# Optimization experiments

Hardware: AMD Instinct MI355X
Metric: run time of the kernel (lower is better)

The kernel has to match this reference:

```python
import jax, jax.numpy as jnp
import numpy as np

NUM_AGENT = 200
LOOK_BACK = 10
NUM_CTRL = 9
DIM = 512
HEADS = 8
DIM_HEAD = 64
N = NUM_AGENT * LOOK_BACK + NUM_CTRL  # 2009
BATCH = 4
SCALE = DIM_HEAD ** -0.5


def _build_mask():
    # eye(num_agent) repeat_interleaved by look_back on rows and cols == kron with ones(lb,lb)
    m = jnp.kron(jnp.eye(NUM_AGENT, dtype=jnp.float32),
                 jnp.ones((LOOK_BACK, LOOK_BACK), jnp.float32))
    # pad with zeros for the control-feature rows/cols
    return jnp.pad(m, ((0, NUM_CTRL), (0, NUM_CTRL)))  # [N, N]


def _split_heads(t):
    b, n, hd = t.shape
    return t.reshape(b, n, HEADS, hd // HEADS).transpose(0, 2, 1, 3)  # [b,h,n,d]


def setup_inputs() -> dict:
    key = jax.random.key(0)
    ks = jax.random.split(key, 5)
    inner = HEADS * DIM_HEAD
    return {
        "x": jax.random.normal(ks[0], (BATCH, N, DIM), jnp.float32),
        "w_qkv": jax.random.normal(ks[1], (DIM, inner * 3), jnp.float32) * 0.02,
        "w_qk_self": jax.random.normal(ks[2], (DIM, inner * 2), jnp.float32) * 0.02,
        "w_out": jax.random.normal(ks[3], (inner, DIM), jnp.float32) * 0.02,
        "b_out": jnp.zeros((DIM,), jnp.float32),
    }


def reference(x, w_qkv, w_qk_self, w_out, b_out):
    mask = _build_mask()  # [N, N], broadcasts over [b, h]
    q, k, v = map(_split_heads, jnp.split(x @ w_qkv, 3, axis=-1))
    q_s, k_s = map(_split_heads, jnp.split(x @ w_qk_self, 2, axis=-1))
    dots = jnp.einsum('bhnd,bhmd->bhnm', q, k) * SCALE
    dots_self = jnp.einsum('bhnd,bhmd->bhnm', q_s, k_s) * SCALE
    blended = mask * dots_self + (1.0 - mask) * dots
    attn = jax.nn.softmax(blended, axis=-1)  # [b,h,n,n]
    out = jnp.einsum('bhnm,bhmd->bhnd', attn, v)
    out = out.transpose(0, 2, 1, 3).reshape(x.shape[0], N, HEADS * DIM_HEAD)
    return out @ w_out + b_out, attn
```

## Files before the change

### kernel.cpp

```cpp
#include <hip/hip_runtime.h>
#include <hip/hip_bf16.h>


#define N_TOK   2009
#define NPAD    2048
#define NTILES  16
#define NT2     32
#define BATCH_  4
#define HEADS_  8
#define MROWS   8036
#define SCALE_  0.125f
#define RPB_A   256
#define RPV     128
#define PFP     68

typedef __attribute__((ext_vector_type(8)))  short sh8;
typedef __attribute__((ext_vector_type(16))) float f32x16;

static inline int cdiv(int a, int b) { return (a + b - 1) / b; }

__device__ __forceinline__ float4 ld4(const float* p) {
    return *reinterpret_cast<const float4*>(p);
}
__device__ __forceinline__ unsigned short f2bf(float f) {
    __hip_bfloat16 h = __float2bfloat16(f);
    return *reinterpret_cast<unsigned short*>(&h);
}
__device__ __forceinline__ float bf2f(unsigned short u) {
    return __uint_as_float(((unsigned)u) << 16);
}
__device__ __forceinline__ void cvt8(const float4& a, const float4& b, sh8& hi, sh8& lo) {
    float f[8] = {a.x, a.y, a.z, a.w, b.x, b.y, b.z, b.w};
#pragma unroll
    for (int i = 0; i < 8; ++i) {
        unsigned short h = f2bf(f[i]);
        hi[i] = (short)h;
        lo[i] = (short)f2bf(f[i] - bf2f(h));
    }
}
__device__ __forceinline__ void cvt8p(const float4& a, const float4& b, sh8& hi) {
#pragma unroll
    for (int i = 0; i < 4; ++i) {
        hi[i]     = (short)f2bf((&a.x)[i]);
        hi[4 + i] = (short)f2bf((&b.x)[i]);
    }
}
typedef const __attribute__((address_space(1))) void gas_void;
typedef __attribute__((address_space(3))) void las_void;
__device__ __forceinline__ void gll16(const void* g, void* l) {
    __builtin_amdgcn_global_load_lds((gas_void*)g, (las_void*)l, 16, 0, 0);
}

__device__ __forceinline__ void bar_lds() {
    asm volatile("s_waitcnt lgkmcnt(0)" ::: "memory");
    __builtin_amdgcn_sched_barrier(0);
    __builtin_amdgcn_s_barrier();
    __builtin_amdgcn_sched_barrier(0);
}
__device__ __forceinline__ void bar_keep16() {
    asm volatile("s_waitcnt vmcnt(16) lgkmcnt(0)" ::: "memory");
    __builtin_amdgcn_sched_barrier(0);
    __builtin_amdgcn_s_barrier();
    __builtin_amdgcn_sched_barrier(0);
}

__global__ __launch_bounds__(256)
void convert_x(const float* __restrict__ x, unsigned short* __restrict__ xh,
               unsigned short* __restrict__ xl)
{
    const int mt = blockIdx.x;
    const int yq = blockIdx.y;
    const int w  = threadIdx.x >> 6;
    const int kc = threadIdx.x & 63;
    for (int it = 0; it < 2; ++it) {
        int rg = (yq * 2 + it) * 4 + w;
        sh8 hi[4], lo[4];
#pragma unroll
        for (int rr = 0; rr < 4; ++rr) {
            int row = rg * 4 + rr;
            int gm = mt * 128 + row;
            int b = gm >> 11, gr = gm & 2047;
            float4 a = make_float4(0.f, 0.f, 0.f, 0.f), c = a;
            if (gr < N_TOK) {
                const float* p = x + ((size_t)b * N_TOK + gr) * 512 + kc * 8;
                a = ld4(p); c = ld4(p + 4);
            }
            cvt8(a, c, hi[rr], lo[rr]);
        }
        size_t base = ((size_t)(mt * 64 + kc) * 128 + rg * 4) * 8;
#pragma unroll
        for (int rr = 0; rr < 4; ++rr) {
            *reinterpret_cast<sh8*>(xh + base + rr * 8) = hi[rr];
            *reinterpret_cast<sh8*>(xl + base + rr * 8) = lo[rr];
        }
    }
}

__global__ __launch_bounds__(256)
void convert_w(const float* __restrict__ wqkv, const float* __restrict__ wself,
               const float* __restrict__ wout,
               unsigned short* __restrict__ qh, unsigned short* __restrict__ ql,
               unsigned short* __restrict__ sh, unsigned short* __restrict__ sl,
               unsigned short* __restrict__ oh, unsigned short* __restrict__ ol)
{
    int cid = blockIdx.x * 256 + threadIdx.x;
    int nt_all = cid >> 13, rem = cid & 8191;
    int kc = rem >> 7, col = rem & 127;
    const float* src; unsigned short *dh, *dl; int Nn, ntl;
    if (nt_all < 12)      { src = wqkv;  dh = qh; dl = ql; Nn = 1536; ntl = nt_all; }
    else if (nt_all < 20) { src = wself; dh = sh; dl = sl; Nn = 1024; ntl = nt_all - 12; }
    else                  { src = wout;  dh = oh; dl = ol; Nn = 512;  ntl = nt_all - 20; }
    float f[8];
#pragma unroll
    for (int i = 0; i < 8; ++i)
        f[i] = src[(size_t)(kc * 8 + i) * Nn + ntl * 128 + col];
    sh8 hi, lo;
    cvt8(make_float4(f[0], f[1], f[2], f[3]), make_float4(f[4], f[5], f[6], f[7]), hi, lo);
    size_t off = ((size_t)(ntl * 64 + kc) * 128 + col) * 8;
    *reinterpret_cast<sh8*>(dh + off) = hi;
    *reinterpret_cast<sh8*>(dl + off) = lo;
}

template<int MODE>
__global__ __launch_bounds__(512)
void gemm_bf16(const unsigned short* __restrict__ Ah, const unsigned short* __restrict__ Al,
               const unsigned short* __restrict__ Bh, const unsigned short* __restrict__ Bl,
               float* __restrict__ C, const float* __restrict__ bias)
{
    __shared__ __align__(16) unsigned short AhS[2][4096], AlS[2][4096],
                                            BhS[2][4096], BlS[2][4096];
    const int tid = threadIdx.x, lane = tid & 63, wid = tid >> 6;
    const int mt = blockIdx.x, ntile = blockIdx.y;
    const int wm = wid >> 2, wn = wid & 3;
    const int lj = lane & 31, g = lane >> 5;

    const unsigned short* Asrc_h = Ah + (size_t)mt * 65536;
    const unsigned short* Asrc_l = Al + (size_t)mt * 65536;
    const unsigned short* Bsrc_h = Bh + (size_t)ntile * 65536;
    const unsigned short* Bsrc_l = Bl + (size_t)ntile * 65536;

#define GSTAGE(BUF, S) do {                                                      \
    gll16(Asrc_h + (size_t)(S) * 4096 + tid * 8, (char*)AhS[BUF] + tid * 16);    \
    gll16(Asrc_l + (size_t)(S) * 4096 + tid * 8, (char*)AlS[BUF] + tid * 16);    \
    gll16(Bsrc_h + (size_t)(S) * 4096 + tid * 8, (char*)BhS[BUF] + tid * 16);    \
    gll16(Bsrc_l + (size_t)(S) * 4096 + tid * 8, (char*)BlS[BUF] + tid * 16);    \
} while (0)

    f32x16 acc[2];
#pragma unroll
    for (int i = 0; i < 16; ++i) { acc[0][i] = 0.f; acc[1][i] = 0.f; }

    GSTAGE(0, 0);
    for (int s = 0; s < 16; ++s) {
        const int buf = s & 1;
        __syncthreads();
        if (s + 1 < 16) GSTAGE(buf ^ 1, s + 1);
#pragma unroll
        for (int ks = 0; ks < 2; ++ks) {
            const int kcl = 2 * ks + g;
            sh8 bh = *reinterpret_cast<const sh8*>(BhS[buf] + (kcl * 128 + wn * 32 + lj) * 8);
            sh8 bl = *reinterpret_cast<const sh8*>(BlS[buf] + (kcl * 128 + wn * 32 + lj) * 8);
#pragma unroll
            for (int Mt = 0; Mt < 2; ++Mt) {
                sh8 ah = *reinterpret_cast<const sh8*>(AhS[buf] + (kcl * 128 + wm * 64 + Mt * 32 + lj) * 8);
                sh8 al = *reinterpret_cast<const sh8*>(AlS[buf] + (kcl * 128 + wm * 64 + Mt * 32 + lj) * 8);
                acc[Mt] = __builtin_amdgcn_mfma_f32_32x32x16_bf16(ah, bh, acc[Mt], 0, 0, 0);
                acc[Mt] = __builtin_amdgcn_mfma_f32_32x32x16_bf16(ah, bl, acc[Mt], 0, 0, 0);
                acc[Mt] = __builtin_amdgcn_mfma_f32_32x32x16_bf16(al, bh, acc[Mt], 0, 0, 0);
            }
        }
    }
#undef GSTAGE

#pragma unroll
    for (int Mt = 0; Mt < 2; ++Mt) {
#pragma unroll
        for (int reg = 0; reg < 16; ++reg) {
            int rloc = wm * 64 + Mt * 32 + (reg & 3) + 8 * (reg >> 2) + 4 * g;
            int gm = mt * 128 + rloc;
            int b = gm >> 11, gr = gm & 2047;
            if (gr < N_TOK) {
                int coln = ntile * 128 + wn * 32 + lj;
                float v = acc[Mt][reg];
                size_t idx;
                if (MODE == 1)
                    idx = ((size_t)(coln >> 9) * MROWS + (size_t)b * N_TOK + gr) * 512 + (coln & 511);
                else if (MODE == 0)
                    idx = ((size_t)b * N_TOK + gr) * 1024 + coln;
                else {
                    v += bias[coln];
                    idx = ((size_t)b * N_TOK + gr) * 512 + coln;
                }
                C[idx] = v;
            }
        }
    }
}

__global__ __launch_bounds__(256)
void selfE_k(const float* __restrict__ proj2, float* __restrict__ selfE)
{
    __shared__ float qs[10][64];
    __shared__ float ks[10][68];
    const int a = blockIdx.x;
    const int h = blockIdx.y & 7;
    const int b = blockIdx.y >> 3;
    const size_t rowbase = (size_t)b * N_TOK + a * 10;

    for (int i = threadIdx.x; i < 320; i += 256) {
        int r = i >> 4;
        int c = (i & 15) * 4;
        const float* src = proj2 + (rowbase + (r % 10)) * 1024
                         + (r < 10 ? 0 : 512) + h * 64 + c;
        float4 v = ld4(src);
        if (r < 10) *reinterpret_cast<float4*>(&qs[r][c]) = v;
        else        *reinterpret_cast<float4*>(&ks[r - 10][c]) = v;
    }
    __syncthreads();
    if (threadIdx.x < 100) {
        int r = threadIdx.x / 10, c = threadIdx.x % 10;
        float acc = 0.f;
#pragma unroll 8
        for (int d = 0; d < 64; ++d) acc += qs[r][d] * ks[c][d];
        int bh = b * HEADS_ + h;
        selfE[((size_t)bh * 2000 + a * 10 + r) * 10 + c] = __expf(acc * SCALE_);
    }
}

__global__ __launch_bounds__(256)
void convert_kv(const float* __restrict__ Kf, const float* __restrict__ Vf,
                unsigned short* __restrict__ Khg, unsigned short* __restrict__ Klg,
                unsigned short* __restrict__ Vtg)
{
    __shared__ float vtile[128][66];
    const int t  = blockIdx.x;
    const int h  = blockIdx.y & 7;
    const int b  = blockIdx.y >> 3;
    const int bh = blockIdx.y;
    const size_t bN = (size_t)b * N_TOK;
    const size_t tbase = ((size_t)bh * NTILES + t) * 8192;
    const int tid = threadIdx.x;

    {
        int r = tid >> 1, q = tid & 1;
        int gj = t * 128 + r;
        float4 f[8];
        if (gj < N_TOK) {
            const float* kp = Kf + (bN + gj) * 512 + h * 64 + q * 32;
#pragma unroll
            for (int i = 0; i < 8; ++i) f[i] = ld4(kp + 4 * i);
        } else {
#pragma unroll
            for (int i = 0; i < 8; ++i) f[i] = make_float4(0.f, 0.f, 0.f, 0.f);
        }
#pragma unroll
        for (int cp = 0; cp < 4; ++cp) {
            sh8 hi, lo;
            cvt8(f[2 * cp], f[2 * cp + 1], hi, lo);
            int kc = q * 4 + cp;
            size_t off = tbase + ((size_t)kc * 128 + r) * 8;
            *reinterpret_cast<sh8*>(Khg + off) = hi;
            *reinterpret_cast<sh8*>(Klg + off) = lo;
        }
    }
    {
        int r = tid >> 1, q = tid & 1;
        int gj = t * 128 + r;
        const float* vp = Vf + (bN + gj) * 512 + h * 64 + q * 32;
#pragma unroll
        for (int i = 0; i < 8; ++i) {
            float4 v = (gj < N_TOK) ? ld4(vp + 4 * i) : make_float4(0.f, 0.f, 0.f, 0.f);
            *reinterpret_cast<float4*>(&vtile[r][q * 32 + 4 * i]) = v;
        }
    }
    __syncthreads();
    {
        int d = tid & 63, jg = tid >> 6;
#pragma unroll
        for (int jj = 0; jj < 4; ++jj) {
            int jc = jg * 4 + jj;
            sh8 pk;
#pragma unroll
            for (int i = 0; i < 8; ++i) pk[i] = (short)f2bf(vtile[jc * 8 + i][d]);
            *reinterpret_cast<sh8*>(Vtg + tbase + ((size_t)jc * 64 + d) * 8) = pk;
        }
    }
}

__global__ __launch_bounds__(512, 2)
void attn_rowsum(const float* __restrict__ Qf,
                 const unsigned short* __restrict__ Khg,
                 const float* __restrict__ selfE,
                 float* __restrict__ rowinv)
{
    __shared__ __align__(16) unsigned short KhS[2][8192];
    __shared__ float selfS[RPB_A * 10];

    const int bid = blockIdx.x;
    const int xcd = bid & 7, idx = bid >> 3;
    const int bh  = xcd * 4 + (idx >> 3);
    const int bx  = idx & 7;
    const int h = bh & 7, b = bh >> 3;
    const int tid = threadIdx.x, lane = tid & 63, wid = tid >> 6;
    const int row0 = bx * RPB_A;
    const int wr = wid * 32;
    const size_t bN = (size_t)b * N_TOK;
    const int lj = lane & 31, g = lane >> 5;

    for (int i = tid; i < RPB_A * 10; i += 512) {
        int r = i / 10, c = i - r * 10;
        int gr = row0 + r;
        selfS[i] = (gr < 2000) ? selfE[((size_t)bh * 2000 + gr) * 10 + c] : 0.f;
    }

    sh8 qh[4];
    {
        int grow = row0 + wr + lj;
        bool val = grow < N_TOK;
        const float* qp = Qf + (bN + (val ? grow : 0)) * 512 + h * 64;
#pragma unroll
        for (int ks = 0; ks < 4; ++ks) {
            int kc = 2 * ks + g;
            float4 a = val ? ld4(qp + kc * 8)     : make_float4(0.f, 0.f, 0.f, 0.f);
            float4 c = val ? ld4(qp + kc * 8 + 4) : make_float4(0.f, 0.f, 0.f, 0.f);
            cvt8p(a, c, qh[ks]);
        }
    }

    const unsigned short* ktiles = Khg + (size_t)bh * NTILES * 8192;
#define RSTAGE(T) do {                                                          \
    const unsigned short* kt = ktiles + (size_t)(T) * 8192;                     \
    char* dst = (char*)KhS[(T) & 1];                                            \
    _Pragma("unroll") for (int i = 0; i < 2; ++i)                               \
        gll16(kt + i * 4096 + tid * 8, dst + i * 8192 + tid * 16); } while (0)

    RSTAGE(0);

    float rsacc[16];
#pragma unroll
    for (int i = 0; i < 16; ++i) rsacc[i] = 0.f;

    const int alo = (row0 / 10) * 10;
    const int rmax = row0 + RPB_A - 1 < 1999 ? row0 + RPB_A - 1 : 1999;
    const int ahi = (rmax / 10) * 10 + 10;

    for (int t = 0; t < NTILES; ++t) {
        __syncthreads();
        if (t + 1 < NTILES) RSTAGE(t + 1);
        const unsigned short* kb = KhS[t & 1];
        const bool dtile = (alo < t * 128 + 128) && (ahi > t * 128);
#pragma unroll
        for (int ct = 0; ct < 4; ++ct) {
            sh8 kf[4];
#pragma unroll
            for (int ks = 0; ks < 4; ++ks)
                kf[ks] = *reinterpret_cast<const sh8*>(kb + ((2 * ks + g) * 128 + 32 * ct + lj) * 8);
            f32x16 s;
#pragma unroll
            for (int i = 0; i < 16; ++i) s[i] = 0.f;
#pragma unroll
            for (int ks = 0; ks < 4; ++ks)
                s = __builtin_amdgcn_mfma_f32_32x32x16_bf16(qh[ks], kf[ks], s, 0, 0, 0);
            const int gj = t * 128 + 32 * ct + lj;
            if (gj < N_TOK) {
#pragma unroll
                for (int reg = 0; reg < 16; ++reg) {
                    int rloc = wr + (reg & 3) + 8 * (reg >> 2) + 4 * g;
                    int grow = row0 + rloc;
                    float e = __expf(s[reg] * SCALE_);
                    if (dtile && grow < 2000) {
                        int a0 = (grow / 10) * 10;
                        unsigned cc = (unsigned)(gj - a0);
                        if (cc < 10u) e = selfS[rloc * 10 + (int)cc];
                    }
                    rsacc[reg] += e;
                }
            }
        }
    }
#undef RSTAGE

#pragma unroll
    for (int reg = 0; reg < 16; ++reg) {
        float v = rsacc[reg];
        v += __shfl_xor(v, 1);  v += __shfl_xor(v, 2);
        v += __shfl_xor(v, 4);  v += __shfl_xor(v, 8);
        v += __shfl_xor(v, 16);
        rsacc[reg] = v;
    }
    if (lj == 0) {
#pragma unroll
        for (int reg = 0; reg < 16; ++reg) {
            int rloc = wr + (reg & 3) + 8 * (reg >> 2) + 4 * g;
            int grow = row0 + rloc;
            rowinv[(size_t)bh * NPAD + row0 + rloc] =
                (grow < N_TOK) ? 1.0f / rsacc[reg] : 0.f;
        }
    }
}

__global__ __launch_bounds__(512, 2)
void attn_pv(const float* __restrict__ Qf,
             const unsigned short* __restrict__ Khg,
             const unsigned short* __restrict__ Klg,
             const unsigned short* __restrict__ Vtg,
             const float* __restrict__ selfE,
             const float* __restrict__ rowinv,
             float* __restrict__ attn,
             unsigned short* __restrict__ Ohg, unsigned short* __restrict__ Olg,
             float* __restrict__ dump)
{
    extern __shared__ __align__(16) char smem[];
    unsigned short* KhS = (unsigned short*)smem;
    unsigned short* KlS = KhS + 4096;
    unsigned short* VtS = KlS + 4096;
    float* Pf = (float*)(VtS + 8192);
    unsigned short* selfS = (unsigned short*)(Pf + RPV * PFP);
    float* rinvS = (float*)(selfS + RPV * 10);

    const int bid = blockIdx.x;
    const int xcd = bid & 7, idx = bid >> 3;
    const int bh  = xcd * 4 + (idx >> 4);
    const int bx  = idx & 15;
    const int h = bh & 7, b = bh >> 3;
    const int tid = threadIdx.x, lane = tid & 63, wid = tid >> 6;
    const int row0 = bx * RPV;
    const int wr = (wid & 3) * 32;
    const int cw = wid >> 2;
    const size_t bN = (size_t)b * N_TOK;
    const size_t abase = ((size_t)bh * N_TOK + row0) * N_TOK;
    const int lj = lane & 31, g = lane >> 5;
    float* dumpT = dump + ((size_t)(bid & 511) << 6) + lane;

    for (int i = tid; i < RPV * 10; i += 512) {
        int r = i / 10, c = i - r * 10;
        int gr = row0 + r;
        selfS[i] = (gr < 2000) ? f2bf(selfE[((size_t)bh * 2000 + gr) * 10 + c]) : 0;
    }
    if (tid < RPV) rinvS[tid] = rowinv[(size_t)bh * NPAD + row0 + tid];

    sh8 qh[4], ql[4];
    {
        int grow = row0 + wr + lj;
        bool val = grow < N_TOK;
        const float* qp = Qf + (bN + (val ? grow : 0)) * 512 + h * 64;
#pragma unroll
        for (int ks = 0; ks < 4; ++ks) {
            int kc = 2 * ks + g;
            float4 a = val ? ld4(qp + kc * 8)     : make_float4(0.f, 0.f, 0.f, 0.f);
            float4 c = val ? ld4(qp + kc * 8 + 4) : make_float4(0.f, 0.f, 0.f, 0.f);
            cvt8(a, c, qh[ks], ql[ks]);
        }
    }

    const unsigned short* khT = Khg + (size_t)bh * NTILES * 8192;
    const unsigned short* klT = Klg + (size_t)bh * NTILES * 8192;
    const unsigned short* vtT = Vtg + (size_t)bh * NTILES * 8192;

#define STAGE_KH(T) gll16(khT + (size_t)((T) >> 1) * 8192                           \
        + ((size_t)(tid >> 6) * 128 + 64 * ((T) & 1) + (tid & 63)) * 8,             \
        (char*)KhS + tid * 16)
#define STAGE_KL(T) gll16(klT + (size_t)((T) >> 1) * 8192                           \
        + ((size_t)(tid >> 6) * 128 + 64 * ((T) & 1) + (tid & 63)) * 8,             \
        (char*)KlS + tid * 16)
#define STAGE_VT(T) gll16(vtT + (size_t)((T) >> 1) * 8192                           \
        + ((size_t)(8 * ((T) & 1) + (tid >> 6)) * 64 + (tid & 63)) * 8,             \
        (char*)(VtS + ((T) & 1) * 4096) + tid * 16)

#define QK_PHASE(T) do {                                                            \
        const bool dtile = (alo < (T) * 64 + 64) && (ahi > (T) * 64);               \
        sh8 kfh[4], kfl[4];                                                         \
        _Pragma("unroll") for (int ks = 0; ks < 4; ++ks) {                          \
            int off = ((2 * ks + g) * 64 + 32 * cw + lj) * 8;                       \
            kfh[ks] = *reinterpret_cast<const sh8*>(KhS + off);                     \
            kfl[ks] = *reinterpret_cast<const sh8*>(KlS + off);                     \
        }                                                                           \
        f32x16 s;                                                                   \
        _Pragma("unroll") for (int i = 0; i < 16; ++i) s[i] = 0.f;                  \
        _Pragma("unroll") for (int ks = 0; ks < 4; ++ks) {                          \
            s = __builtin_amdgcn_mfma_f32_32x32x16_bf16(qh[ks], kfh[ks], s, 0,0,0); \
            s = __builtin_amdgcn_mfma_f32_32x32x16_bf16(qh[ks], kfl[ks], s, 0,0,0); \
            s = __builtin_amdgcn_mfma_f32_32x32x16_bf16(ql[ks], kfh[ks], s, 0,0,0); \
        }                                                                           \
        const int cin = 32 * cw + lj;                                               \
        const int gj  = (T) * 64 + cin;                                             \
        const bool jv = gj < N_TOK;                                                 \
        _Pragma("unroll") for (int reg = 0; reg < 16; ++reg) {                      \
            int rowl = (reg & 3) + 8 * (reg >> 2) + 4 * g;                          \
            int rloc = wr + rowl;                                                   \
            int grow = row0 + rloc;                                                 \
            float e = 0.f;                                                          \
            if (jv && grow < N_TOK) e = __expf(s[reg] * SCALE_);                    \
            if (dtile && jv && grow < 2000) {                                       \
                int a0 = (grow / 10) * 10;                                          \
                unsigned cc = (unsigned)(gj - a0);                                  \
                if (cc < 10u) e = bf2f(selfS[rloc * 10 + (int)cc]);                 \
            }                                                                       \
            Pf[rloc * PFP + cin] = e * rinvS[rloc];                                 \
        }                                                                           \
    } while (0)

#define PV_PHASE(T) do {                                                            \
        const unsigned short* vtb = VtS + ((T) & 1) * 4096;                         \
        _Pragma("unroll") for (int m = 0; m < 4; ++m) {                             \
            const float* pp = &Pf[(wr + lj) * PFP + 16 * m + 8 * g];                \
            float4 a = ld4(pp), b4 = ld4(pp + 4);                                   \
            sh8 pa; cvt8p(a, b4, pa);                                               \
            sh8 vf = *reinterpret_cast<const sh8*>(                                 \
                vtb + ((2 * m + g) * 64 + 32 * cw + lj) * 8);                       \
            oacc = __builtin_amdgcn_mfma_f32_32x32x16_bf16(pa, vf, oacc, 0, 0, 0);  \
        }                                                                           \
    } while (0)

    STAGE_KH(0); STAGE_KL(0); STAGE_VT(0);

    const int alo = (row0 / 10) * 10;
    const int rmax = row0 + RPV - 1 < 1999 ? row0 + RPV - 1 : 1999;
    const int ahi = (rmax / 10) * 10 + 10;

    f32x16 oacc;
#pragma unroll
    for (int i = 0; i < 16; ++i) oacc[i] = 0.f;

    __syncthreads();

    const int rbase = wid * 16;

    for (int t = 0; t < NT2 - 1; ++t) {
        QK_PHASE(t);
        bar_lds();
        STAGE_KH(t + 1); STAGE_KL(t + 1); STAGE_VT(t + 1);
        {
            float* ap0 = attn + abase + (size_t)t * 64 + lane;
#pragma unroll
            for (int i = 0; i < 16; ++i) {
                int r = rbase + i;
                int grow = row0 + r;
                float v = Pf[r * PFP + lane];
                float* sdst = (grow < N_TOK) ? (ap0 + (size_t)r * N_TOK) : dumpT;
                *sdst = v;
            }
        }
        PV_PHASE(t);
        bar_keep16();
    }

    {
        const int t = NT2 - 1;
        QK_PHASE(t);
        __syncthreads();
        PV_PHASE(t);
        if (t * 64 + lane < N_TOK) {
            float* ap0 = attn + abase + (size_t)t * 64 + lane;
#pragma unroll
            for (int i = 0; i < 16; ++i) {
                int r = rbase + i;
                int grow = row0 + r;
                if (grow < N_TOK)
                    ap0[(size_t)r * N_TOK] = Pf[r * PFP + lane];
            }
        }
        __syncthreads();
    }
#undef STAGE_KH
#undef STAGE_KL
#undef STAGE_VT
#undef QK_PHASE
#undef PV_PHASE

    float* Ofull = (float*)smem;
#pragma unroll
    for (int reg = 0; reg < 16; ++reg) {
        int rloc = wr + (reg & 3) + 8 * (reg >> 2) + 4 * g;
        Ofull[rloc * 68 + 32 * cw + lj] = oacc[reg];
    }
    __syncthreads();
#pragma unroll
    for (int it = 0; it < 2; ++it) {
        int task = it * 512 + tid;
        int row = task >> 3, kq = task & 7;
        const float* op = Ofull + row * 68 + kq * 8;
        float4 a = ld4(op), c = ld4(op + 4);
        sh8 hi, lo; cvt8(a, c, hi, lo);
        int gm = b * 2048 + row0 + row;
        int mtile = gm >> 7, row128 = gm & 127;
        size_t off = ((size_t)(mtile * 64 + h * 8 + kq) * 128 + row128) * 8;
        *reinterpret_cast<sh8*>(Ohg + off) = hi;
        *reinterpret_cast<sh8*>(Olg + off) = lo;
    }
}

extern "C" void kernel_launch(void* const* d_in, const int* in_sizes, int n_in,
                              void* d_out, int out_size, void* d_ws, size_t ws_size,
                              hipStream_t stream)
{
    const float* x         = (const float*)d_in[0];
    const float* w_qkv     = (const float*)d_in[1];
    const float* w_qk_self = (const float*)d_in[2];
    const float* w_out     = (const float*)d_in[3];
    const float* b_out     = (const float*)d_in[4];

    float* out  = (float*)d_out;
    float* attn = out + (size_t)MROWS * 512;

    float* Qf = (float*)d_ws;
    float* Kf = Qf + (size_t)MROWS * 512;
    float* Vf = Kf + (size_t)MROWS * 512;
    float* p2 = Vf + (size_t)MROWS * 512;
    unsigned short* Khg = (unsigned short*)p2;
    unsigned short* Klg = Khg + 4194304;
    unsigned short* Vtg = Klg + 4194304;
    float* proj2 = p2;
    float* after_p2 = p2 + (size_t)MROWS * 1024;
    unsigned short* xh  = (unsigned short*)after_p2;
    unsigned short* xl  = xh + 4194304;
    unsigned short* Wqh = xl + 4194304;
    unsigned short* Wql = Wqh + 786432;
    unsigned short* Wsh = Wql + 786432;
    unsigned short* Wsl = Wsh + 524288;
    unsigned short* Woh = Wsl + 524288;
    unsigned short* Wol = Woh + 262144;
    float* rowinv = (float*)(Wol + 262144);
    float* selfE  = rowinv + 65536;
    float* dump   = selfE + 640000;
    unsigned short* Ohg = (unsigned short*)Kf;
    unsigned short* Olg = Ohg + 4194304;

    const int smem_pv = 8192 + 8192 + 16384
                      + RPV * PFP * 4
                      + RPV * 10 * 2 + RPV * 4;
    hipFuncSetAttribute((const void*)attn_pv,
                        hipFuncAttributeMaxDynamicSharedMemorySize, smem_pv);

    dim3 gx(64, 4);
    convert_x<<<gx, 256, 0, stream>>>(x, xh, xl);
    convert_w<<<768, 256, 0, stream>>>(w_qkv, w_qk_self, w_out,
                                       Wqh, Wql, Wsh, Wsl, Woh, Wol);

    dim3 g1(64, 12);
    gemm_bf16<1><<<g1, 512, 0, stream>>>(xh, xl, Wqh, Wql, Qf, nullptr);

    dim3 g2(64, 8);
    gemm_bf16<0><<<g2, 512, 0, stream>>>(xh, xl, Wsh, Wsl, proj2, nullptr);

    dim3 gs(200, 32);
    selfE_k<<<gs, 256, 0, stream>>>(proj2, selfE);

    dim3 gc(NTILES, 32);
    convert_kv<<<gc, 256, 0, stream>>>(Kf, Vf, Khg, Klg, Vtg);

    attn_rowsum<<<256, 512, 0, stream>>>(Qf, Khg, selfE, rowinv);

    attn_pv<<<512, 512, smem_pv, stream>>>(Qf, Khg, Klg, Vtg, selfE, rowinv,
                                           attn, Ohg, Olg, dump);

    dim3 g3(64, 4);
    gemm_bf16<2><<<g3, 512, 0, stream>>>(Ohg, Olg, Woh, Wol, out, b_out);
}
```

Measured before the change: 469.5 us.

## Halve attn_pv row tile to 64 and use 256-thread blocks with 3 per CU

Shrinks the rows per attn_pv block from 128 to 64, so each block has 4 waves (2 row groups x 2 column groups) instead of 8 and the grid doubles to 1024 blocks. The K/V staging macros are rewritten so 256 threads issue two loads each to fill the same LDS tiles. The XCD-aware block-to-(bh,row) mapping and the dump indexing are adjusted to match. The aim is better occupancy and load balance across CUs, at the cost of staging each K/V tile twice as often per output row, which means more LDS and global traffic per unit of work.

```diff
diff --git a/kernel.cpp b/kernel.cpp
--- a/kernel.cpp
+++ b/kernel.cpp
@@ -11,7 +11,7 @@
 #define MROWS   8036
 #define SCALE_  0.125f
 #define RPB_A   256
-#define RPV     128
+#define RPV     64
 #define PFP     68
 
 typedef __attribute__((ext_vector_type(8)))  short sh8;
@@ -399,7 +399,7 @@
     }
 }
 
-__global__ __launch_bounds__(512, 2)
+__global__ __launch_bounds__(256, 3)
 void attn_pv(const float* __restrict__ Qf,
              const unsigned short* __restrict__ Khg,
              const unsigned short* __restrict__ Klg,
@@ -419,20 +419,20 @@
     float* rinvS = (float*)(selfS + RPV * 10);
 
     const int bid = blockIdx.x;
-    const int xcd = bid & 7, idx = bid >> 3;
-    const int bh  = xcd * 4 + (idx >> 4);
-    const int bx  = idx & 15;
+    const int xcd = bid & 7, sub = bid >> 3;
+    const int bh  = xcd * 4 + (sub >> 5);
+    const int bx  = sub & 31;
     const int h = bh & 7, b = bh >> 3;
     const int tid = threadIdx.x, lane = tid & 63, wid = tid >> 6;
     const int row0 = bx * RPV;
-    const int wr = (wid & 3) * 32;
-    const int cw = wid >> 2;
+    const int wr = (wid & 1) * 32;
+    const int cw = wid >> 1;
     const size_t bN = (size_t)b * N_TOK;
     const size_t abase = ((size_t)bh * N_TOK + row0) * N_TOK;
     const int lj = lane & 31, g = lane >> 5;
-    float* dumpT = dump + ((size_t)(bid & 511) << 6) + lane;
-
-    for (int i = tid; i < RPV * 10; i += 512) {
+    float* dumpT = dump + ((size_t)bid << 6) + lane;
+
+    for (int i = tid; i < RPV * 10; i += 256) {
         int r = i / 10, c = i - r * 10;
         int gr = row0 + r;
         selfS[i] = (gr < 2000) ? f2bf(selfE[((size_t)bh * 2000 + gr) * 10 + c]) : 0;
@@ -457,15 +457,25 @@
     const unsigned short* klT = Klg + (size_t)bh * NTILES * 8192;
     const unsigned short* vtT = Vtg + (size_t)bh * NTILES * 8192;
 
-#define STAGE_KH(T) gll16(khT + (size_t)((T) >> 1) * 8192                           \
-        + ((size_t)(tid >> 6) * 128 + 64 * ((T) & 1) + (tid & 63)) * 8,             \
-        (char*)KhS + tid * 16)
-#define STAGE_KL(T) gll16(klT + (size_t)((T) >> 1) * 8192                           \
-        + ((size_t)(tid >> 6) * 128 + 64 * ((T) & 1) + (tid & 63)) * 8,             \
-        (char*)KlS + tid * 16)
-#define STAGE_VT(T) gll16(vtT + (size_t)((T) >> 1) * 8192                           \
-        + ((size_t)(8 * ((T) & 1) + (tid >> 6)) * 64 + (tid & 63)) * 8,             \
-        (char*)(VtS + ((T) & 1) * 4096) + tid * 16)
+#define STAGE_KH(T) do { const unsigned short* src = khT + (size_t)((T) >> 1) * 8192 \
+        + 512 * ((T) & 1);                                                           \
+    _Pragma("unroll") for (int r_ = 0; r_ < 2; ++r_) {                               \
+        int s_ = tid + 256 * r_;                                                     \
+        gll16(src + ((s_ >> 6) * 1024 + (s_ & 63) * 8), (char*)KhS + s_ * 16);       \
+    } } while (0)
+#define STAGE_KL(T) do { const unsigned short* src = klT + (size_t)((T) >> 1) * 8192 \
+        + 512 * ((T) & 1);                                                           \
+    _Pragma("unroll") for (int r_ = 0; r_ < 2; ++r_) {                               \
+        int s_ = tid + 256 * r_;                                                     \
+        gll16(src + ((s_ >> 6) * 1024 + (s_ & 63) * 8), (char*)KlS + s_ * 16);       \
+    } } while (0)
+#define STAGE_VT(T) do { const unsigned short* src = vtT + (size_t)((T) >> 1) * 8192 \
+        + 4096 * ((T) & 1);                                                          \
+    char* dst = (char*)VtS + ((T) & 1) * 8192;                                       \
+    _Pragma("unroll") for (int r_ = 0; r_ < 2; ++r_) {                               \
+        int s_ = tid + 256 * r_;                                                     \
+        gll16(src + s_ * 8, dst + s_ * 16);                                          \
+    } } while (0)
 
 #define QK_PHASE(T) do {                                                            \
         const bool dtile = (alo < (T) * 64 + 64) && (ahi > (T) * 64);               \
@@ -577,7 +587,7 @@
     __syncthreads();
 #pragma unroll
     for (int it = 0; it < 2; ++it) {
-        int task = it * 512 + tid;
+        int task = it * 256 + tid;
         int row = task >> 3, kq = task & 7;
         const float* op = Ofull + row * 68 + kq * 8;
         float4 a = ld4(op), c = ld4(op + 4);
@@ -651,8 +661,8 @@
 
     attn_rowsum<<<256, 512, 0, stream>>>(Qf, Khg, selfE, rowinv);
 
-    attn_pv<<<512, 512, smem_pv, stream>>>(Qf, Khg, Klg, Vtg, selfE, rowinv,
-                                           attn, Ohg, Olg, dump);
+    attn_pv<<<1024, 256, smem_pv, stream>>>(Qf, Khg, Klg, Vtg, selfE, rowinv,
+                                            attn, Ohg, Olg, dump);
 
     dim3 g3(64, 4);
     gemm_bf16<2><<<g3, 512, 0, stream>>>(Ohg, Olg, Woh, Wol, out, b_out);
```

After: 510.4 us. 1.09x slower.

## Add dedicated store waves to attn_pv for attention matrix writeback

Applied to the files above, without the earlier changes.

Grows the attn_pv block from 8 to 12 waves. Eight compute waves run the QK, softmax and PV MFMA phases while four extra waves write the 128x64 probability tile from shared memory to the global attn output. The two groups hand off each tile through block barriers, so the large attn stores are meant to overlap compute instead of sitting inside the compute waves' loop. In exchange the compute waves now wait for vmcnt(0) on every iteration, which drops the previous partial-wait overlap of prefetches. The launch bound (768,6) also asks for a register budget that may force spills or cut occupancy.

```diff
diff --git a/kernel.cpp b/kernel.cpp
--- a/kernel.cpp
+++ b/kernel.cpp
@@ -51,14 +51,14 @@
     __builtin_amdgcn_global_load_lds((gas_void*)g, (las_void*)l, 16, 0, 0);
 }
 
-__device__ __forceinline__ void bar_lds() {
+__device__ __forceinline__ void bar_lgkm() {
     asm volatile("s_waitcnt lgkmcnt(0)" ::: "memory");
     __builtin_amdgcn_sched_barrier(0);
     __builtin_amdgcn_s_barrier();
     __builtin_amdgcn_sched_barrier(0);
 }
-__device__ __forceinline__ void bar_keep16() {
-    asm volatile("s_waitcnt vmcnt(16) lgkmcnt(0)" ::: "memory");
+__device__ __forceinline__ void bar_vm_lgkm() {
+    asm volatile("s_waitcnt vmcnt(0) lgkmcnt(0)" ::: "memory");
     __builtin_amdgcn_sched_barrier(0);
     __builtin_amdgcn_s_barrier();
     __builtin_amdgcn_sched_barrier(0);
@@ -399,7 +399,7 @@
     }
 }
 
-__global__ __launch_bounds__(512, 2)
+__global__ __launch_bounds__(768, 6)
 void attn_pv(const float* __restrict__ Qf,
              const unsigned short* __restrict__ Khg,
              const unsigned short* __restrict__ Klg,
@@ -407,8 +407,7 @@
              const float* __restrict__ selfE,
              const float* __restrict__ rowinv,
              float* __restrict__ attn,
-             unsigned short* __restrict__ Ohg, unsigned short* __restrict__ Olg,
-             float* __restrict__ dump)
+             unsigned short* __restrict__ Ohg, unsigned short* __restrict__ Olg)
 {
     extern __shared__ __align__(16) char smem[];
     unsigned short* KhS = (unsigned short*)smem;
@@ -425,14 +424,14 @@
     const int h = bh & 7, b = bh >> 3;
     const int tid = threadIdx.x, lane = tid & 63, wid = tid >> 6;
     const int row0 = bx * RPV;
-    const int wr = (wid & 3) * 32;
-    const int cw = wid >> 2;
     const size_t bN = (size_t)b * N_TOK;
     const size_t abase = ((size_t)bh * N_TOK + row0) * N_TOK;
     const int lj = lane & 31, g = lane >> 5;
-    float* dumpT = dump + ((size_t)(bid & 511) << 6) + lane;
-
-    for (int i = tid; i < RPV * 10; i += 512) {
+    const bool is_compute = (wid < 8);
+    const int wr = (wid & 3) * 32;
+    const int cw = (wid >> 2) & 1;
+
+    for (int i = tid; i < RPV * 10; i += 768) {
         int r = i / 10, c = i - r * 10;
         int gr = row0 + r;
         selfS[i] = (gr < 2000) ? f2bf(selfE[((size_t)bh * 2000 + gr) * 10 + c]) : 0;
@@ -440,7 +439,7 @@
     if (tid < RPV) rinvS[tid] = rowinv[(size_t)bh * NPAD + row0 + tid];
 
     sh8 qh[4], ql[4];
-    {
+    if (is_compute) {
         int grow = row0 + wr + lj;
         bool val = grow < N_TOK;
         const float* qp = Qf + (bN + (val ? grow : 0)) * 512 + h * 64;
@@ -512,8 +511,6 @@
         }                                                                           \
     } while (0)
 
-    STAGE_KH(0); STAGE_KL(0); STAGE_VT(0);
-
     const int alo = (row0 / 10) * 10;
     const int rmax = row0 + RPV - 1 < 1999 ? row0 + RPV - 1 : 1999;
     const int ahi = (rmax / 10) * 10 + 10;
@@ -522,45 +519,36 @@
 #pragma unroll
     for (int i = 0; i < 16; ++i) oacc[i] = 0.f;
 
-    __syncthreads();
-
-    const int rbase = wid * 16;
-
-    for (int t = 0; t < NT2 - 1; ++t) {
-        QK_PHASE(t);
-        bar_lds();
-        STAGE_KH(t + 1); STAGE_KL(t + 1); STAGE_VT(t + 1);
-        {
-            float* ap0 = attn + abase + (size_t)t * 64 + lane;
-#pragma unroll
-            for (int i = 0; i < 16; ++i) {
-                int r = rbase + i;
-                int grow = row0 + r;
-                float v = Pf[r * PFP + lane];
-                float* sdst = (grow < N_TOK) ? (ap0 + (size_t)r * N_TOK) : dumpT;
-                *sdst = v;
+    if (is_compute) {
+        STAGE_KH(0); STAGE_KL(0); STAGE_VT(0);
+        bar_vm_lgkm();
+        for (int t = 0; t < NT2; ++t) {
+            QK_PHASE(t);
+            bar_lgkm();
+            if (t + 1 < NT2) { STAGE_KH(t + 1); STAGE_KL(t + 1); STAGE_VT(t + 1); }
+            PV_PHASE(t);
+            bar_vm_lgkm();
+        }
+    } else {
+        const int sw = wid - 8;
+        bar_lgkm();
+        for (int t = 0; t < NT2; ++t) {
+            __builtin_amdgcn_s_barrier();
+            __builtin_amdgcn_sched_barrier(0);
+            {
+                const int gj = t * 64 + lane;
+                const bool colv = gj < N_TOK;
+                float* ap0 = attn + abase + gj;
+#pragma unroll 8
+                for (int i = 0; i < 32; ++i) {
+                    int r = sw * 32 + i;
+                    float v = Pf[r * PFP + lane];
+                    if (colv && (row0 + r) < N_TOK)
+                        ap0[(size_t)r * N_TOK] = v;
+                }
             }
-        }
-        PV_PHASE(t);
-        bar_keep16();
-    }
-
-    {
-        const int t = NT2 - 1;
-        QK_PHASE(t);
-        __syncthreads();
-        PV_PHASE(t);
-        if (t * 64 + lane < N_TOK) {
-            float* ap0 = attn + abase + (size_t)t * 64 + lane;
-#pragma unroll
-            for (int i = 0; i < 16; ++i) {
-                int r = rbase + i;
-                int grow = row0 + r;
-                if (grow < N_TOK)
-                    ap0[(size_t)r * N_TOK] = Pf[r * PFP + lane];
-            }
-        }
-        __syncthreads();
+            bar_lgkm();
+        }
     }
 #undef STAGE_KH
 #undef STAGE_KL
@@ -568,16 +556,17 @@
 #undef QK_PHASE
 #undef PV_PHASE
 
+    __syncthreads();
     float* Ofull = (float*)smem;
-#pragma unroll
-    for (int reg = 0; reg < 16; ++reg) {
-        int rloc = wr + (reg & 3) + 8 * (reg >> 2) + 4 * g;
-        Ofull[rloc * 68 + 32 * cw + lj] = oacc[reg];
+    if (is_compute) {
+#pragma unroll
+        for (int reg = 0; reg < 16; ++reg) {
+            int rloc = wr + (reg & 3) + 8 * (reg >> 2) + 4 * g;
+            Ofull[rloc * 68 + 32 * cw + lj] = oacc[reg];
+        }
     }
     __syncthreads();
-#pragma unroll
-    for (int it = 0; it < 2; ++it) {
-        int task = it * 512 + tid;
+    for (int task = tid; task < 1024; task += 768) {
         int row = task >> 3, kq = task & 7;
         const float* op = Ofull + row * 68 + kq * 8;
         float4 a = ld4(op), c = ld4(op + 4);
@@ -622,7 +611,6 @@
     unsigned short* Wol = Woh + 262144;
     float* rowinv = (float*)(Wol + 262144);
     float* selfE  = rowinv + 65536;
-    float* dump   = selfE + 640000;
     unsigned short* Ohg = (unsigned short*)Kf;
     unsigned short* Olg = Ohg + 4194304;
 
@@ -651,8 +639,8 @@
 
     attn_rowsum<<<256, 512, 0, stream>>>(Qf, Khg, selfE, rowinv);
 
-    attn_pv<<<512, 512, smem_pv, stream>>>(Qf, Khg, Klg, Vtg, selfE, rowinv,
-                                           attn, Ohg, Olg, dump);
+    attn_pv<<<512, 768, smem_pv, stream>>>(Qf, Khg, Klg, Vtg, selfE, rowinv,
+                                           attn, Ohg, Olg);
 
     dim3 g3(64, 4);
     gemm_bf16<2><<<g3, 512, 0, stream>>>(Ohg, Olg, Woh, Wol, out, b_out);
```

After: 746.5 us. 59.0% more time.
